# Kernel tuning notes

Measured on AMD Instinct MI355X. Metric: run time of the kernel, lower is better.

Reference implementation:

```python
import jax, jax.numpy as jnp
import numpy as np

N, E, IN_DIM, HID, OUT = 50000, 800000, 128, 128, 64


def setup_inputs() -> dict:
    key = jax.random.key(0)
    k = jax.random.split(key, 6)
    h = jax.random.normal(k[0], (N, IN_DIM), dtype=jnp.float32)
    edge_index = jax.random.randint(k[1], (2, E), 0, N, dtype=jnp.int64)
    s_in, s_hid = 1.0 / np.sqrt(IN_DIM), 1.0 / np.sqrt(HID)
    W_gcn = jax.random.uniform(k[2], (IN_DIM, HID), jnp.float32, -s_in, s_in)
    b_gcn = jnp.zeros((HID,), jnp.float32)
    W_fc = jax.random.uniform(k[3], (HID, OUT), jnp.float32, -s_hid, s_hid)
    b_fc = jax.random.uniform(k[4], (OUT,), jnp.float32, -s_hid, s_hid)
    return {"h": h, "edge_index": edge_index, "W_gcn": W_gcn,
            "b_gcn": b_gcn, "W_fc": W_fc, "b_fc": b_fc}


def reference(h, edge_index, W_gcn, b_gcn, W_fc, b_fc):
    n = h.shape[0]
    # GCNConv: transform, add self-loops, symmetric normalization, scatter-add
    x = h @ W_gcn                                   # [N, HID]
    loop = jnp.arange(n, dtype=edge_index.dtype)
    row = jnp.concatenate([edge_index[0], loop])    # source nodes
    col = jnp.concatenate([edge_index[1], loop])    # destination nodes
    deg = jax.ops.segment_sum(jnp.ones_like(col, dtype=x.dtype), col,
                              num_segments=n)       # in-degree incl. self-loop
    dinv = jnp.where(deg > 0, jax.lax.rsqrt(deg), 0.0)
    norm = dinv[row] * dinv[col]                    # [E+N]
    msg = x[row] * norm[:, None]                    # gather + scale
    agg = jax.ops.segment_sum(msg, col, num_segments=n) + b_gcn
    # ReLU then projection
    return jax.nn.relu(agg) @ W_fc + b_fc
```

## Files before the change

kernel.cpp:

```cpp
#include <hip/hip_runtime.h>

#define N_NODES 50000
#define N_EDGES 800000
#define TOT (N_EDGES + N_NODES)
#define NBKT 196
#define BCAP 6144

typedef __attribute__((ext_vector_type(4))) float floatx4;
typedef __attribute__((ext_vector_type(8))) _Float16 half8;
typedef __attribute__((ext_vector_type(2))) _Float16 half2v;

#define O_PTR   0UL
#define O_GF    200192UL
#define O_CB    201216UL
#define O_FLAG  202240UL
#define O_DINV  202496UL
#define O_ESRC  402688UL
#define O_W1    3802880UL
#define O_W2    3835648UL
#define O_XS    3852032UL
#define O_YR    16652032UL

__global__ void k_prep(const float* __restrict__ Wg, const float* __restrict__ Wf,
                       const unsigned* __restrict__ ei_raw,
                       int* gfill, _Float16* W1, _Float16* W2, int* flags) {
    int i = blockIdx.x * 256 + threadIdx.x;
    if (i < 128 * 128) { int n = i >> 7, k = i & 127; W1[i] = (_Float16)Wg[k * 128 + n]; }
    if (i < 64 * 128)  { int n = i >> 7, k = i & 127; W2[i] = (_Float16)Wf[k * 64 + n]; }
    if (i < NBKT) gfill[i] = 0;
    if (i >= 16320) {
        int lane = i - 16320;
        unsigned w = ei_raw[2 * lane + 1];
        unsigned long long m = __ballot(w == 0u);
        if (lane == 0) flags[1] = (__popcll(m) >= 60) ? 1 : 0;
    }
}

__global__ __launch_bounds__(256) void k_binA(const int* __restrict__ ei,
                                              const int* __restrict__ flags,
                                              int* __restrict__ gfill,
                                              unsigned* __restrict__ staging) {
    __shared__ int cnt[NBKT];
    __shared__ int gbase[NBKT];
    int t = threadIdx.x;
    for (int i = t; i < NBKT; i += 256) cnt[i] = 0;
    __syncthreads();
    int ebase = blockIdx.x * 4096;
    bool i64 = flags[1] != 0;
    unsigned pk[16]; int rk[16]; short bk[16];
#pragma unroll
    for (int j = 0; j < 16; ++j) {
        int e = ebase + j * 256 + t;
        if (e < N_EDGES) {
            int s, d;
            if (i64) { s = ei[2 * e]; d = ei[2 * (N_EDGES + e)]; }
            else     { s = ei[e];     d = ei[N_EDGES + e]; }
            int b = d >> 8;
            bk[j] = (short)b;
            pk[j] = (unsigned)s | ((unsigned)(d & 255) << 16);
            rk[j] = atomicAdd(&cnt[b], 1);
        } else bk[j] = -1;
    }
    __syncthreads();
    for (int i = t; i < NBKT; i += 256)
        gbase[i] = atomicAdd(&gfill[i], cnt[i]);
    __syncthreads();
#pragma unroll
    for (int j = 0; j < 16; ++j) {
        if (bk[j] >= 0) {
            int pos = gbase[bk[j]] + rk[j];
            if (pos < BCAP) staging[(size_t)bk[j] * BCAP + pos] = pk[j];
        }
    }
}

__global__ void k_scanB(const int* __restrict__ gfill, int* __restrict__ cbase) {
    __shared__ int sm[256];
    int t = threadIdx.x;
    int nn = (t < NBKT) ? ((t == NBKT - 1) ? (N_NODES - 256 * (NBKT - 1)) : 256) : 0;
    int v = (t < NBKT) ? (gfill[t] + nn) : 0;
    sm[t] = v; __syncthreads();
    for (int off = 1; off < 256; off <<= 1) {
        int x = (t >= off) ? sm[t - off] : 0;
        __syncthreads(); sm[t] += x; __syncthreads();
    }
    if (t < NBKT) cbase[t] = sm[t] - v;
}

__global__ __launch_bounds__(256) void k_binB(const unsigned* __restrict__ staging,
                                              const int* __restrict__ gfill,
                                              const int* __restrict__ cbase,
                                              int* __restrict__ ptr,
                                              float* __restrict__ dinv,
                                              int* __restrict__ esrc) {
    __shared__ int lcnt[256];
    __shared__ int lscan[256];
    __shared__ int cur[256];
    int b = blockIdx.x;
    int t = threadIdx.x;
    int nbase = b * 256;
    int nn = min(256, N_NODES - nbase);
    int cnt = min(gfill[b], BCAP);
    int cb = cbase[b];
    const unsigned* st = staging + (size_t)b * BCAP;
    lcnt[t] = 0;
    __syncthreads();
    for (int i = t; i < cnt; i += 256)
        atomicAdd(&lcnt[st[i] >> 16], 1);
    __syncthreads();
    int v = lcnt[t];
    lscan[t] = v;
    __syncthreads();
    for (int off = 1; off < 256; off <<= 1) {
        int x = (t >= off) ? lscan[t - off] : 0;
        __syncthreads(); lscan[t] += x; __syncthreads();
    }
    int segstart = cb + (lscan[t] - v) + t;
    if (t < nn) {
        int node = nbase + t;
        ptr[node] = segstart;
        dinv[node] = rsqrtf((float)(v + 1));
        esrc[segstart] = node;
        cur[t] = segstart + 1;
    }
    __syncthreads();
    for (int i = t; i < cnt; i += 256) {
        unsigned p = st[i];
        int pos = atomicAdd(&cur[p >> 16], 1);
        esrc[pos] = (int)(p & 0xffffu);
    }
}

__global__ __launch_bounds__(256) void k_gemm1(const float* __restrict__ h,
                                               const _Float16* __restrict__ W1,
                                               const float* __restrict__ dinv,
                                               _Float16* __restrict__ xs) {
    int wave = threadIdx.x >> 6;
    int lane = threadIdx.x & 63;
    int rowbase = (blockIdx.x * 4 + wave) * 16;
    if (rowbase >= N_NODES) return;
    int quad = lane >> 4;
    int mrow = rowbase + (lane & 15);
    int mr = mrow < N_NODES ? mrow : N_NODES - 1;
    half8 a[4];
#pragma unroll
    for (int kk = 0; kk < 4; ++kk) {
        const floatx4* p = (const floatx4*)(h + (size_t)mr * 128 + kk * 32 + quad * 8);
        floatx4 x0 = p[0], x1 = p[1];
        half8 tt;
#pragma unroll
        for (int j = 0; j < 4; ++j) { tt[j] = (_Float16)x0[j]; tt[4 + j] = (_Float16)x1[j]; }
        a[kk] = tt;
    }
    float dv[4];
#pragma unroll
    for (int i = 0; i < 4; ++i) {
        int r = rowbase + quad * 4 + i;
        dv[i] = (r < N_NODES) ? dinv[r] : 0.f;
    }
#pragma unroll
    for (int nt = 0; nt < 8; ++nt) {
        floatx4 acc = {0.f, 0.f, 0.f, 0.f};
        int n = nt * 16 + (lane & 15);
#pragma unroll
        for (int kk = 0; kk < 4; ++kk) {
            half8 bb = *(const half8*)(W1 + n * 128 + kk * 32 + quad * 8);
            acc = __builtin_amdgcn_mfma_f32_16x16x32_f16(a[kk], bb, acc, 0, 0, 0);
        }
#pragma unroll
        for (int i = 0; i < 4; ++i) {
            int r = rowbase + quad * 4 + i;
            if (r < N_NODES) xs[(size_t)r * 128 + n] = (_Float16)(acc[i] * dv[i]);
        }
    }
}

__global__ __launch_bounds__(256) void k_agg(const _Float16* __restrict__ xs,
                                             const int* __restrict__ ptr,
                                             const int* __restrict__ esrc,
                                             const float* __restrict__ dinv,
                                             const float* __restrict__ bg,
                                             _Float16* __restrict__ yr) {
    int wid = (blockIdx.x * 256 + threadIdx.x) >> 6;
    int lane = threadIdx.x & 63;
    if (wid >= N_NODES) return;
    int p0 = ptr[wid];
    int p1 = (wid + 1 < N_NODES) ? ptr[wid + 1] : TOT;
    float a0 = 0.f, a1 = 0.f;
    for (int base = p0; base < p1; base += 64) {
        int cnt = p1 - base; if (cnt > 64) cnt = 64;
        int idx = 0;
        if (lane < cnt) idx = esrc[base + lane];
        int j = 0;
        for (; j + 4 <= cnt; j += 4) {
            int s0 = __shfl(idx, j);
            int s1 = __shfl(idx, j + 1);
            int s2 = __shfl(idx, j + 2);
            int s3 = __shfl(idx, j + 3);
            half2v u0 = *(const half2v*)(xs + (size_t)s0 * 128 + lane * 2);
            half2v u1 = *(const half2v*)(xs + (size_t)s1 * 128 + lane * 2);
            half2v u2 = *(const half2v*)(xs + (size_t)s2 * 128 + lane * 2);
            half2v u3 = *(const half2v*)(xs + (size_t)s3 * 128 + lane * 2);
            a0 += (float)u0[0] + (float)u1[0] + (float)u2[0] + (float)u3[0];
            a1 += (float)u0[1] + (float)u1[1] + (float)u2[1] + (float)u3[1];
        }
        for (; j < cnt; ++j) {
            int s = __shfl(idx, j);
            half2v u = *(const half2v*)(xs + (size_t)s * 128 + lane * 2);
            a0 += (float)u[0]; a1 += (float)u[1];
        }
    }
    float sc = dinv[wid];
    float r0 = fmaxf(fmaf(a0, sc, bg[lane * 2]), 0.f);
    float r1 = fmaxf(fmaf(a1, sc, bg[lane * 2 + 1]), 0.f);
    half2v o; o[0] = (_Float16)r0; o[1] = (_Float16)r1;
    *(half2v*)(yr + (size_t)wid * 128 + lane * 2) = o;
}

__global__ __launch_bounds__(256) void k_gemm2(const _Float16* __restrict__ yr,
                                               const _Float16* __restrict__ W2,
                                               const float* __restrict__ bfc,
                                               float* __restrict__ out) {
    int wave = threadIdx.x >> 6;
    int lane = threadIdx.x & 63;
    int rowbase = (blockIdx.x * 4 + wave) * 16;
    if (rowbase >= N_NODES) return;
    int quad = lane >> 4;
    int mrow = rowbase + (lane & 15);
    int mr = mrow < N_NODES ? mrow : N_NODES - 1;
    half8 a[4];
#pragma unroll
    for (int kk = 0; kk < 4; ++kk)
        a[kk] = *(const half8*)(yr + (size_t)mr * 128 + kk * 32 + quad * 8);
#pragma unroll
    for (int nt = 0; nt < 4; ++nt) {
        floatx4 acc = {0.f, 0.f, 0.f, 0.f};
        int n = nt * 16 + (lane & 15);
#pragma unroll
        for (int kk = 0; kk < 4; ++kk) {
            half8 bb = *(const half8*)(W2 + n * 128 + kk * 32 + quad * 8);
            acc = __builtin_amdgcn_mfma_f32_16x16x32_f16(a[kk], bb, acc, 0, 0, 0);
        }
        float bias = bfc[n];
#pragma unroll
        for (int i = 0; i < 4; ++i) {
            int r = rowbase + quad * 4 + i;
            if (r < N_NODES) out[(size_t)r * 64 + n] = acc[i] + bias;
        }
    }
}

extern "C" void kernel_launch(void* const* d_in, const int* in_sizes, int n_in,
                              void* d_out, int out_size, void* d_ws, size_t ws_size,
                              hipStream_t stream) {
    (void)in_sizes; (void)n_in; (void)out_size; (void)ws_size;
    const float* h  = (const float*)d_in[0];
    const int*   ei = (const int*)d_in[1];
    const float* Wg = (const float*)d_in[2];
    const float* bg = (const float*)d_in[3];
    const float* Wf = (const float*)d_in[4];
    const float* bf = (const float*)d_in[5];
    float* out = (float*)d_out;

    char* ws = (char*)d_ws;
    int*      ptr   = (int*)(ws + O_PTR);
    int*      gfill = (int*)(ws + O_GF);
    int*      cbase = (int*)(ws + O_CB);
    int*      flags = (int*)(ws + O_FLAG);
    float*    dinv  = (float*)(ws + O_DINV);
    int*      esrc  = (int*)(ws + O_ESRC);
    _Float16* W1    = (_Float16*)(ws + O_W1);
    _Float16* W2    = (_Float16*)(ws + O_W2);
    _Float16* xs    = (_Float16*)(ws + O_XS);
    _Float16* yr    = (_Float16*)(ws + O_YR);
    unsigned* staging = (unsigned*)(ws + O_XS);

    k_prep<<<64, 256, 0, stream>>>(Wg, Wf, (const unsigned*)ei, gfill, W1, W2, flags);
    k_binA<<<NBKT, 256, 0, stream>>>(ei, flags, gfill, staging);
    k_scanB<<<1, 256, 0, stream>>>(gfill, cbase);
    k_binB<<<NBKT, 256, 0, stream>>>(staging, gfill, cbase, ptr, dinv, esrc);
    k_gemm1<<<(N_NODES + 63) / 64, 256, 0, stream>>>(h, W1, dinv, xs);
    k_agg<<<(N_NODES + 3) / 4, 256, 0, stream>>>(xs, ptr, esrc, dinv, bg, yr);
    k_gemm2<<<(N_NODES + 63) / 64, 256, 0, stream>>>(yr, W2, bf, out);
}
```

Before: 177.7 us.

## Aggregate raw features before GEMM and fuse both GEMMs into one kernel

Reorders the GCN as (A·H)·W instead of A·(H·W). Both have the same 128-wide rows, so the gather cost stays the same, but the separate gemm1 pass and its intermediate write go away. The scaled fp16 copy of h is now produced inside k_binB, and the scan kernel is replaced by a per-block prefix sum over gfill. Edge writes are grouped by source range in seven passes to improve locality of the later gathers. The two GEMMs are fused through LDS, which adds passes over the shared staging buffer and a 16 KB LDS footprint per block.

```diff
diff --git a/kernel.cpp b/kernel.cpp
--- a/kernel.cpp
+++ b/kernel.cpp
@@ -12,14 +12,13 @@
 
 #define O_PTR   0UL
 #define O_GF    200192UL
-#define O_CB    201216UL
-#define O_FLAG  202240UL
-#define O_DINV  202496UL
-#define O_ESRC  402688UL
-#define O_W1    3802880UL
-#define O_W2    3835648UL
-#define O_XS    3852032UL
-#define O_YR    16652032UL
+#define O_FLAG  201216UL
+#define O_DINV  201472UL
+#define O_ESRC  401664UL
+#define O_W1    3801856UL
+#define O_W2    3834624UL
+#define O_U     3851008UL
+#define O_H16   16651008UL
 
 __global__ void k_prep(const float* __restrict__ Wg, const float* __restrict__ Wf,
                        const unsigned* __restrict__ ei_raw,
@@ -74,39 +73,39 @@
     }
 }
 
-__global__ void k_scanB(const int* __restrict__ gfill, int* __restrict__ cbase) {
-    __shared__ int sm[256];
-    int t = threadIdx.x;
-    int nn = (t < NBKT) ? ((t == NBKT - 1) ? (N_NODES - 256 * (NBKT - 1)) : 256) : 0;
-    int v = (t < NBKT) ? (gfill[t] + nn) : 0;
-    sm[t] = v; __syncthreads();
-    for (int off = 1; off < 256; off <<= 1) {
-        int x = (t >= off) ? sm[t - off] : 0;
-        __syncthreads(); sm[t] += x; __syncthreads();
-    }
-    if (t < NBKT) cbase[t] = sm[t] - v;
-}
-
 __global__ __launch_bounds__(256) void k_binB(const unsigned* __restrict__ staging,
                                               const int* __restrict__ gfill,
-                                              const int* __restrict__ cbase,
+                                              const float* __restrict__ h,
                                               int* __restrict__ ptr,
                                               float* __restrict__ dinv,
+                                              _Float16* __restrict__ h16,
                                               int* __restrict__ esrc) {
+    __shared__ unsigned se[BCAP];
     __shared__ int lcnt[256];
     __shared__ int lscan[256];
     __shared__ int cur[256];
-    int b = blockIdx.x;
-    int t = threadIdx.x;
+    __shared__ float sdinv[256];
+    __shared__ int s_cb;
+    int b = blockIdx.x, t = threadIdx.x;
     int nbase = b * 256;
     int nn = min(256, N_NODES - nbase);
     int cnt = min(gfill[b], BCAP);
-    int cb = cbase[b];
+    if (t < 64) {
+        int acc = 0;
+        for (int i = t; i < b; i += 64) acc += min(gfill[i], BCAP) + 256;
+#pragma unroll
+        for (int off = 32; off > 0; off >>= 1) acc += __shfl_down(acc, off);
+        if (t == 0) s_cb = acc;
+    }
+    lcnt[t] = 0;
+    __syncthreads();
+    int cb = s_cb;
     const unsigned* st = staging + (size_t)b * BCAP;
-    lcnt[t] = 0;
-    __syncthreads();
-    for (int i = t; i < cnt; i += 256)
-        atomicAdd(&lcnt[st[i] >> 16], 1);
+    for (int i = t; i < cnt; i += 256) {
+        unsigned p = st[i];
+        se[i] = p;
+        atomicAdd(&lcnt[p >> 16], 1);
+    }
     __syncthreads();
     int v = lcnt[t];
     lscan[t] = v;
@@ -116,71 +115,40 @@
         __syncthreads(); lscan[t] += x; __syncthreads();
     }
     int segstart = cb + (lscan[t] - v) + t;
+    float dv = rsqrtf((float)(v + 1));
     if (t < nn) {
         int node = nbase + t;
         ptr[node] = segstart;
-        dinv[node] = rsqrtf((float)(v + 1));
+        dinv[node] = dv;
+        sdinv[t] = dv;
         esrc[segstart] = node;
         cur[t] = segstart + 1;
     }
     __syncthreads();
-    for (int i = t; i < cnt; i += 256) {
-        unsigned p = st[i];
-        int pos = atomicAdd(&cur[p >> 16], 1);
-        esrc[pos] = (int)(p & 0xffffu);
-    }
-}
-
-__global__ __launch_bounds__(256) void k_gemm1(const float* __restrict__ h,
-                                               const _Float16* __restrict__ W1,
-                                               const float* __restrict__ dinv,
-                                               _Float16* __restrict__ xs) {
-    int wave = threadIdx.x >> 6;
-    int lane = threadIdx.x & 63;
-    int rowbase = (blockIdx.x * 4 + wave) * 16;
-    if (rowbase >= N_NODES) return;
-    int quad = lane >> 4;
-    int mrow = rowbase + (lane & 15);
-    int mr = mrow < N_NODES ? mrow : N_NODES - 1;
-    half8 a[4];
-#pragma unroll
-    for (int kk = 0; kk < 4; ++kk) {
-        const floatx4* p = (const floatx4*)(h + (size_t)mr * 128 + kk * 32 + quad * 8);
-        floatx4 x0 = p[0], x1 = p[1];
-        half8 tt;
-#pragma unroll
-        for (int j = 0; j < 4; ++j) { tt[j] = (_Float16)x0[j]; tt[4 + j] = (_Float16)x1[j]; }
-        a[kk] = tt;
-    }
-    float dv[4];
-#pragma unroll
-    for (int i = 0; i < 4; ++i) {
-        int r = rowbase + quad * 4 + i;
-        dv[i] = (r < N_NODES) ? dinv[r] : 0.f;
-    }
-#pragma unroll
-    for (int nt = 0; nt < 8; ++nt) {
-        floatx4 acc = {0.f, 0.f, 0.f, 0.f};
-        int n = nt * 16 + (lane & 15);
-#pragma unroll
-        for (int kk = 0; kk < 4; ++kk) {
-            half8 bb = *(const half8*)(W1 + n * 128 + kk * 32 + quad * 8);
-            acc = __builtin_amdgcn_mfma_f32_16x16x32_f16(a[kk], bb, acc, 0, 0, 0);
-        }
-#pragma unroll
-        for (int i = 0; i < 4; ++i) {
-            int r = rowbase + quad * 4 + i;
-            if (r < N_NODES) xs[(size_t)r * 128 + n] = (_Float16)(acc[i] * dv[i]);
-        }
-    }
-}
-
-__global__ __launch_bounds__(256) void k_agg(const _Float16* __restrict__ xs,
+    for (int g = 0; g < 7; ++g) {
+        for (int i = t; i < cnt; i += 256) {
+            unsigned p = se[i];
+            int s = (int)(p & 0xffffu);
+            if ((s >> 13) == g) {
+                int pos = atomicAdd(&cur[p >> 16], 1);
+                esrc[pos] = s;
+            }
+        }
+        __syncthreads();
+    }
+    int half = t >> 7;
+    int col = t & 127;
+    for (int r = half; r < nn; r += 2) {
+        int node = nbase + r;
+        h16[(size_t)node * 128 + col] = (_Float16)(h[(size_t)node * 128 + col] * sdinv[r]);
+    }
+}
+
+__global__ __launch_bounds__(256) void k_agg(const _Float16* __restrict__ h16,
                                              const int* __restrict__ ptr,
                                              const int* __restrict__ esrc,
                                              const float* __restrict__ dinv,
-                                             const float* __restrict__ bg,
-                                             _Float16* __restrict__ yr) {
+                                             _Float16* __restrict__ u) {
     int wid = (blockIdx.x * 256 + threadIdx.x) >> 6;
     int lane = threadIdx.x & 63;
     if (wid >= N_NODES) return;
@@ -192,60 +160,99 @@
         int idx = 0;
         if (lane < cnt) idx = esrc[base + lane];
         int j = 0;
+        for (; j + 8 <= cnt; j += 8) {
+            int s0 = __shfl(idx, j),     s1 = __shfl(idx, j + 1);
+            int s2 = __shfl(idx, j + 2), s3 = __shfl(idx, j + 3);
+            int s4 = __shfl(idx, j + 4), s5 = __shfl(idx, j + 5);
+            int s6 = __shfl(idx, j + 6), s7 = __shfl(idx, j + 7);
+            half2v u0 = *(const half2v*)(h16 + (size_t)s0 * 128 + lane * 2);
+            half2v u1 = *(const half2v*)(h16 + (size_t)s1 * 128 + lane * 2);
+            half2v u2 = *(const half2v*)(h16 + (size_t)s2 * 128 + lane * 2);
+            half2v u3 = *(const half2v*)(h16 + (size_t)s3 * 128 + lane * 2);
+            half2v u4 = *(const half2v*)(h16 + (size_t)s4 * 128 + lane * 2);
+            half2v u5 = *(const half2v*)(h16 + (size_t)s5 * 128 + lane * 2);
+            half2v u6 = *(const half2v*)(h16 + (size_t)s6 * 128 + lane * 2);
+            half2v u7 = *(const half2v*)(h16 + (size_t)s7 * 128 + lane * 2);
+            a0 += (float)u0[0] + (float)u1[0] + (float)u2[0] + (float)u3[0]
+                + (float)u4[0] + (float)u5[0] + (float)u6[0] + (float)u7[0];
+            a1 += (float)u0[1] + (float)u1[1] + (float)u2[1] + (float)u3[1]
+                + (float)u4[1] + (float)u5[1] + (float)u6[1] + (float)u7[1];
+        }
         for (; j + 4 <= cnt; j += 4) {
-            int s0 = __shfl(idx, j);
-            int s1 = __shfl(idx, j + 1);
-            int s2 = __shfl(idx, j + 2);
-            int s3 = __shfl(idx, j + 3);
-            half2v u0 = *(const half2v*)(xs + (size_t)s0 * 128 + lane * 2);
-            half2v u1 = *(const half2v*)(xs + (size_t)s1 * 128 + lane * 2);
-            half2v u2 = *(const half2v*)(xs + (size_t)s2 * 128 + lane * 2);
-            half2v u3 = *(const half2v*)(xs + (size_t)s3 * 128 + lane * 2);
+            int s0 = __shfl(idx, j),     s1 = __shfl(idx, j + 1);
+            int s2 = __shfl(idx, j + 2), s3 = __shfl(idx, j + 3);
+            half2v u0 = *(const half2v*)(h16 + (size_t)s0 * 128 + lane * 2);
+            half2v u1 = *(const half2v*)(h16 + (size_t)s1 * 128 + lane * 2);
+            half2v u2 = *(const half2v*)(h16 + (size_t)s2 * 128 + lane * 2);
+            half2v u3 = *(const half2v*)(h16 + (size_t)s3 * 128 + lane * 2);
             a0 += (float)u0[0] + (float)u1[0] + (float)u2[0] + (float)u3[0];
             a1 += (float)u0[1] + (float)u1[1] + (float)u2[1] + (float)u3[1];
         }
         for (; j < cnt; ++j) {
             int s = __shfl(idx, j);
-            half2v u = *(const half2v*)(xs + (size_t)s * 128 + lane * 2);
-            a0 += (float)u[0]; a1 += (float)u[1];
+            half2v uu = *(const half2v*)(h16 + (size_t)s * 128 + lane * 2);
+            a0 += (float)uu[0]; a1 += (float)uu[1];
         }
     }
     float sc = dinv[wid];
-    float r0 = fmaxf(fmaf(a0, sc, bg[lane * 2]), 0.f);
-    float r1 = fmaxf(fmaf(a1, sc, bg[lane * 2 + 1]), 0.f);
-    half2v o; o[0] = (_Float16)r0; o[1] = (_Float16)r1;
-    *(half2v*)(yr + (size_t)wid * 128 + lane * 2) = o;
-}
-
-__global__ __launch_bounds__(256) void k_gemm2(const _Float16* __restrict__ yr,
+    half2v o; o[0] = (_Float16)(a0 * sc); o[1] = (_Float16)(a1 * sc);
+    *(half2v*)(u + (size_t)wid * 128 + lane * 2) = o;
+}
+
+__global__ __launch_bounds__(256) void k_gemmF(const _Float16* __restrict__ u,
+                                               const _Float16* __restrict__ W1,
                                                const _Float16* __restrict__ W2,
+                                               const float* __restrict__ bg,
                                                const float* __restrict__ bfc,
                                                float* __restrict__ out) {
+    __shared__ _Float16 zt[4][16 * 128];
     int wave = threadIdx.x >> 6;
     int lane = threadIdx.x & 63;
     int rowbase = (blockIdx.x * 4 + wave) * 16;
-    if (rowbase >= N_NODES) return;
+    if (rowbase > N_NODES - 16) rowbase = N_NODES - 16;
     int quad = lane >> 4;
-    int mrow = rowbase + (lane & 15);
-    int mr = mrow < N_NODES ? mrow : N_NODES - 1;
+    int l15 = lane & 15;
+    int mr = rowbase + l15;
     half8 a[4];
 #pragma unroll
     for (int kk = 0; kk < 4; ++kk)
-        a[kk] = *(const half8*)(yr + (size_t)mr * 128 + kk * 32 + quad * 8);
-#pragma unroll
-    for (int nt = 0; nt < 4; ++nt) {
+        a[kk] = *(const half8*)(u + (size_t)mr * 128 + kk * 32 + quad * 8);
+    _Float16* z = zt[wave];
+#pragma unroll
+    for (int nt = 0; nt < 8; ++nt) {
         floatx4 acc = {0.f, 0.f, 0.f, 0.f};
-        int n = nt * 16 + (lane & 15);
+        int n = nt * 16 + l15;
+#pragma unroll
+        for (int kk = 0; kk < 4; ++kk) {
+            half8 bb = *(const half8*)(W1 + n * 128 + kk * 32 + quad * 8);
+            acc = __builtin_amdgcn_mfma_f32_16x16x32_f16(a[kk], bb, acc, 0, 0, 0);
+        }
+        float bias = bg[n];
+#pragma unroll
+        for (int i = 0; i < 4; ++i) {
+            int row = quad * 4 + i;
+            z[row * 128 + n] = (_Float16)fmaxf(acc[i] + bias, 0.f);
+        }
+    }
+    __syncthreads();
+    half8 a2[4];
+#pragma unroll
+    for (int kk = 0; kk < 4; ++kk)
+        a2[kk] = *(const half8*)(z + l15 * 128 + kk * 32 + quad * 8);
+#pragma unroll
+    for (int mt = 0; mt < 4; ++mt) {
+        floatx4 acc = {0.f, 0.f, 0.f, 0.f};
+        int n = mt * 16 + l15;
 #pragma unroll
         for (int kk = 0; kk < 4; ++kk) {
             half8 bb = *(const half8*)(W2 + n * 128 + kk * 32 + quad * 8);
-            acc = __builtin_amdgcn_mfma_f32_16x16x32_f16(a[kk], bb, acc, 0, 0, 0);
+            acc = __builtin_amdgcn_mfma_f32_16x16x32_f16(a2[kk], bb, acc, 0, 0, 0);
         }
         float bias = bfc[n];
 #pragma unroll
         for (int i = 0; i < 4; ++i) {
-            int r = rowbase + quad * 4 + i;
-            if (r < N_NODES) out[(size_t)r * 64 + n] = acc[i] + bias;
+            int row = rowbase + quad * 4 + i;
+            out[(size_t)row * 64 + n] = acc[i] + bias;
         }
     }
 }
@@ -265,21 +272,18 @@
     char* ws = (char*)d_ws;
     int*      ptr   = (int*)(ws + O_PTR);
     int*      gfill = (int*)(ws + O_GF);
-    int*      cbase = (int*)(ws + O_CB);
     int*      flags = (int*)(ws + O_FLAG);
     float*    dinv  = (float*)(ws + O_DINV);
     int*      esrc  = (int*)(ws + O_ESRC);
     _Float16* W1    = (_Float16*)(ws + O_W1);
     _Float16* W2    = (_Float16*)(ws + O_W2);
-    _Float16* xs    = (_Float16*)(ws + O_XS);
-    _Float16* yr    = (_Float16*)(ws + O_YR);
-    unsigned* staging = (unsigned*)(ws + O_XS);
+    _Float16* u     = (_Float16*)(ws + O_U);
+    _Float16* h16   = (_Float16*)(ws + O_H16);
+    unsigned* staging = (unsigned*)(ws + O_U);
 
     k_prep<<<64, 256, 0, stream>>>(Wg, Wf, (const unsigned*)ei, gfill, W1, W2, flags);
     k_binA<<<NBKT, 256, 0, stream>>>(ei, flags, gfill, staging);
-    k_scanB<<<1, 256, 0, stream>>>(gfill, cbase);
-    k_binB<<<NBKT, 256, 0, stream>>>(staging, gfill, cbase, ptr, dinv, esrc);
-    k_gemm1<<<(N_NODES + 63) / 64, 256, 0, stream>>>(h, W1, dinv, xs);
-    k_agg<<<(N_NODES + 3) / 4, 256, 0, stream>>>(xs, ptr, esrc, dinv, bg, yr);
-    k_gemm2<<<(N_NODES + 63) / 64, 256, 0, stream>>>(yr, W2, bf, out);
-}
+    k_binB<<<NBKT, 256, 0, stream>>>(staging, gfill, h, ptr, dinv, h16, esrc);
+    k_agg<<<(N_NODES + 3) / 4, 256, 0, stream>>>(h16, ptr, esrc, dinv, u);
+    k_gemmF<<<(N_NODES + 63) / 64, 256, 0, stream>>>(u, W1, W2, bg, bf, out);
+}
```

Result: no change. 180.9 us (+1.8%).
